# Kernel optimization log

Measured on AMD Instinct MI355X. Metric: run time of the kernel, lower is better.

The kernel has to match this reference:

```python
import jax, jax.numpy as jnp
import numpy as np

B, T, C, H = 2, 2048, 1024, 16
NS, NL, STEP = 3, 1, 8            # n_s_token, n_l_token, online_step
NPF = NS + NL                      # tokens per frame
CHUNK = STEP * NPF                 # online chunk size = 32
D = C // H


def _build_causal_mask():
    # Faithful port of the buffer construction in __init__ (host-side numpy).
    m = np.tril(np.ones((T, T), dtype=np.float32))
    step = np.zeros((T, T), dtype=np.float32)
    for i in range(0, T, CHUNK):
        step[i:i + CHUNK, i:i + CHUNK] = 1.0
        for j in range(i, i + CHUNK, NPF):
            m[j + NS:j + NPF, :] = 0.0
            m[:, j + NS:j + NPF] = 0.0
    return jnp.asarray(((m + step) == 0.0))[None, None]  # (1,1,T,T) bool


def setup_inputs() -> dict:
    key = jax.random.key(0)
    ks = jax.random.split(key, 10)
    sc = 0.02
    return {
        "x": jax.random.normal(ks[0], (B, T, C), dtype=jnp.float32),
        "dynamic_mask": jax.random.randint(ks[1], (B, 1, T, T), 0, 2).astype(bool),
        "causal_mask": _build_causal_mask(),
        "Wq": jax.random.normal(ks[2], (C, C), dtype=jnp.float32) * sc,
        "bq": jnp.zeros((C,), dtype=jnp.float32),
        "Wk": jax.random.normal(ks[3], (C, C), dtype=jnp.float32) * sc,
        "bk": jnp.zeros((C,), dtype=jnp.float32),
        "Wv": jax.random.normal(ks[4], (C, C), dtype=jnp.float32) * sc,
        "bv": jnp.zeros((C,), dtype=jnp.float32),
        "Wo": jax.random.normal(ks[5], (C, C), dtype=jnp.float32) * sc,
        "bo": jnp.zeros((C,), dtype=jnp.float32),
    }


def reference(x, dynamic_mask, causal_mask, Wq, bq, Wk, bk, Wv, bv, Wo, bo):
    Bb, Tt, Cc = x.shape
    scale = jnp.asarray(D, x.dtype) ** -0.5
    # nn.Linear: y = x @ W.T + b ; split heads -> (B,H,T,D)
    q = (x @ Wq.T + bq).reshape(Bb, Tt, H, D).transpose(0, 2, 1, 3)
    k = (x @ Wk.T + bk).reshape(Bb, Tt, H, D).transpose(0, 2, 1, 3)
    v = (x @ Wv.T + bv).reshape(Bb, Tt, H, D).transpose(0, 2, 1, 3)
    att = jnp.einsum('bhqd,bhkd->bhqk', q, k) * scale       # (B,H,T,T)
    neg_inf = jnp.asarray(-jnp.inf, att.dtype)
    att = jnp.where(causal_mask, neg_inf, att)
    att = jnp.where(dynamic_mask, neg_inf, att)
    att = jax.nn.softmax(att, axis=-1)                      # attn_drop is identity (eval)
    y = jnp.einsum('bhqk,bhkd->bhqd', att, v)
    y = y.transpose(0, 2, 1, 3).reshape(Bb, Tt, Cc)
    return y @ Wo.T + bo                                    # resid_drop is identity (eval)
```

## Files before the change

### kernel.cpp

```cpp
#include <hip/hip_runtime.h>

#define TSEQ 2048
#define NHEAD 16
#define DHEAD 64
#define CDIM 1024
#define BATCH 2

typedef __attribute__((ext_vector_type(8))) short bfx8;
typedef __attribute__((ext_vector_type(4))) short bfx4;
typedef __attribute__((ext_vector_type(4))) float f32x4;

__device__ __forceinline__ unsigned short f2bf(float f) {
  unsigned u = __builtin_bit_cast(unsigned, f);
  u += 0x7fffu + ((u >> 16) & 1u);
  return (unsigned short)(u >> 16);
}

__device__ __forceinline__ unsigned cvtpk(float lo, float hi) {
  unsigned r;
  asm("v_cvt_pk_bf16_f32 %0, %1, %2" : "=v"(r) : "v"(lo), "v"(hi));
  return r;
}

__device__ __forceinline__ float max3f(float a, float b, float c) {
  float d;
  asm("v_max3_f32 %0, %1, %2, %3" : "=v"(d) : "v"(a), "v"(b), "v"(c));
  return d;
}

__device__ __forceinline__ void gload16(const void* g, void* l) {
  __builtin_amdgcn_global_load_lds(
      (const __attribute__((address_space(1))) unsigned*)g,
      (__attribute__((address_space(3))) unsigned*)l, 16, 0, 0);
}

__global__ __launch_bounds__(256) void prep(
    const float* __restrict__ x,
    const float* __restrict__ wq, const float* __restrict__ wk,
    const float* __restrict__ wv, const float* __restrict__ wo,
    short* __restrict__ xb, short* __restrict__ wall,
    const unsigned char* __restrict__ dyn,
    const unsigned char* __restrict__ causal,
    unsigned long long* __restrict__ pm) {
  const int bid = blockIdx.x;
  if (bid < 20480) {
    const int y = bid >> 12;
    const float* src;
    short* dst;
    int n;
    if (y == 0) { src = x; dst = xb; n = (BATCH * TSEQ * CDIM) / 4; }
    else {
      src = (y == 1) ? wq : (y == 2) ? wk : (y == 3) ? wv : wo;
      dst = wall + (size_t)(y - 1) * CDIM * CDIM;
      n = (CDIM * CDIM) / 4;
    }
    const int i = (bid & 4095) * 256 + threadIdx.x;
    if (i < n) {
      const float4 v = ((const float4*)src)[i];
      bfx4 o;
      o[0] = (short)f2bf(v.x); o[1] = (short)f2bf(v.y);
      o[2] = (short)f2bf(v.z); o[3] = (short)f2bf(v.w);
      ((bfx4*)dst)[i] = o;
    }
  } else {
    const bool mbyte = (causal[32] != 0);
    const int wave = threadIdx.x >> 6, lane = threadIdx.x & 63;
    const int gid = (bid - 20480) * 4 + wave;
    const int tile = gid & 31;
    const int q = (gid >> 5) & (TSEQ - 1);
    const int b = gid >> 16;
    const int g = lane >> 4, blk = (lane >> 2) & 3, r = lane & 3;
    const int k = tile * 64 + blk * 16 + g * 4 + r;
    const size_t off = ((size_t)b * TSEQ + q) * TSEQ + k;
    const bool dm = mbyte ? (dyn[off] != 0) : (((const int*)dyn)[off] != 0);
    const bool qok = (q & 3) != 3;
    const bool al =
        (((k >> 5) == (q >> 5)) || ((k <= q) && qok && (r != 3))) && !dm;
    const unsigned long long bal = __ballot(!al);
    if (lane == 0) pm[gid] = bal;
  }
}

__global__ __launch_bounds__(256) void gemm_qkv(
    const short* __restrict__ A, const short* __restrict__ Ball,
    const float* __restrict__ bias0, const float* __restrict__ bias1,
    const float* __restrict__ bias2,
    short* __restrict__ Oq, short* __restrict__ Ok, short* __restrict__ VT) {
  __shared__ char arena[35072];
  const int bid = blockIdx.x;
  const int xcd = bid & 7, local = bid >> 3;
  const int m_idx = (xcd >> 1) * 8 + (local & 7);
  const int nz = (xcd & 1) * 12 + (local >> 3);
  const int which = nz >> 3, n_idx = nz & 7;
  const int tid = threadIdx.x;
  const int w = tid >> 6, lane = tid & 63;
  const int lq = lane & 15, g = lane >> 4;
  const int wr = w >> 1, wc = w & 1;
  const int m0 = m_idx * 128, n0 = n_idx * 128;
  const short* B = Ball + (size_t)which * CDIM * CDIM;
#define ASB(bi) ((short*)(arena + (bi) * 8192))
#define BSB(bi) ((short*)(arena + 16384 + (bi) * 8192))
#define GS(bi, kt)                                                             \
  {                                                                            \
    _Pragma("unroll") for (int ph = 0; ph < 2; ++ph) {                         \
      const int c = ph * 256 + tid;                                            \
      gload16(A + (size_t)(m0 + (c >> 2)) * CDIM + (kt) * 32 + (c & 3) * 8,    \
              ASB(bi) + (ph * 256 + w * 64) * 8);                              \
      gload16(B + (size_t)(n0 + (c >> 2)) * CDIM + (kt) * 32 + (c & 3) * 8,    \
              BSB(bi) + (ph * 256 + w * 64) * 8);                              \
    }                                                                          \
  }
  GS(0, 0);
  __syncthreads();
  f32x4 acc[4][4] = {};
#pragma unroll 2
  for (int kt = 0; kt < CDIM / 32; ++kt) {
    const int bi = kt & 1;
    if (kt + 1 < CDIM / 32) GS(bi ^ 1, kt + 1);
    bfx8 af[4], bfr[4];
#pragma unroll
    for (int i = 0; i < 4; ++i)
      af[i] = *(const bfx8*)&ASB(bi)[(wr * 64 + i * 16 + lq) * 32 + g * 8];
#pragma unroll
    for (int i = 0; i < 4; ++i)
      bfr[i] = *(const bfx8*)&BSB(bi)[(wc * 64 + i * 16 + lq) * 32 + g * 8];
#pragma unroll
    for (int i = 0; i < 4; ++i)
#pragma unroll
      for (int j = 0; j < 4; ++j)
        acc[i][j] = __builtin_amdgcn_mfma_f32_16x16x32_bf16(af[i], bfr[j],
                                                            acc[i][j], 0, 0, 0);
    __syncthreads();
  }
#undef GS
  const float* bias = (which == 0) ? bias0 : (which == 1) ? bias1 : bias2;
  const float scale = (which == 0) ? 0.18033688011112042f : 1.0f;
  short* tile = (short*)arena;
  const int rs = (which == 2) ? 137 : 136;
#pragma unroll
  for (int i = 0; i < 4; ++i)
#pragma unroll
    for (int j = 0; j < 4; ++j) {
      const int col = wc * 64 + j * 16 + lq;
      const float bb = bias[n0 + col];
#pragma unroll
      for (int r = 0; r < 4; ++r) {
        const int row = wr * 64 + i * 16 + g * 4 + r;
        tile[row * rs + col] = (short)f2bf((acc[i][j][r] + bb) * scale);
      }
    }
  __syncthreads();
  const int b_ = m0 >> 11, t0 = m0 & (TSEQ - 1);
  if (which == 2) {
#pragma unroll
    for (int it = 0; it < 8; ++it) {
      const int id = it * 256 + tid;
      const int tseg = id & 15, d128 = id >> 4;
      const int h = (n0 >> 6) + (d128 >> 6), d = d128 & 63;
      bfx8 o;
#pragma unroll
      for (int j = 0; j < 8; ++j) o[j] = tile[(tseg * 8 + j) * 137 + d128];
      *(bfx8*)&VT[(((size_t)b_ * NHEAD + h) * DHEAD + d) * TSEQ + t0 +
                  tseg * 8] = o;
    }
  } else {
    short* O = (which == 0) ? Oq : Ok;
#pragma unroll
    for (int it = 0; it < 8; ++it) {
      const int id = it * 256 + tid;
      const int m = id >> 4, c16 = id & 15;
      const int h = (n0 >> 6) + (c16 >> 3), d0 = (c16 & 7) * 8;
      *(bfx8*)&O[(((size_t)b_ * NHEAD + h) * TSEQ + t0 + m) * DHEAD + d0] =
          *(const bfx8*)&tile[m * 136 + c16 * 8];
    }
  }
}

__global__ __launch_bounds__(256) void gemm_out(
    const short* __restrict__ A, const short* __restrict__ B,
    const float* __restrict__ bias, float* __restrict__ Of) {
  __shared__ char arena[24576];
  const int bid = blockIdx.x;
  const int xcd = bid & 7, local = bid >> 3;
  const int m_idx = (xcd >> 1) * 16 + (local & 15);
  const int n_idx = (xcd & 1) * 4 + (local >> 4);
  const int tid = threadIdx.x;
  const int w = tid >> 6, lane = tid & 63;
  const int lq = lane & 15, g = lane >> 4;
  const int wr = w >> 1, wc = w & 1;
  const int m0 = m_idx * 64, n0 = n_idx * 128;
#define ASB(bi) ((short*)(arena + (bi) * 4096))
#define BSB(bi) ((short*)(arena + 8192 + (bi) * 8192))
#define GS(bi, kt)                                                             \
  {                                                                            \
    gload16(A + (size_t)(m0 + (tid >> 2)) * CDIM + (kt) * 32 + (tid & 3) * 8,  \
            ASB(bi) + (w * 64) * 8);                                           \
    _Pragma("unroll") for (int ph = 0; ph < 2; ++ph) {                         \
      const int c = ph * 256 + tid;                                            \
      gload16(B + (size_t)(n0 + (c >> 2)) * CDIM + (kt) * 32 + (c & 3) * 8,    \
              BSB(bi) + (ph * 256 + w * 64) * 8);                              \
    }                                                                          \
  }
  GS(0, 0);
  __syncthreads();
  f32x4 acc[2][4] = {};
#pragma unroll 2
  for (int kt = 0; kt < CDIM / 32; ++kt) {
    const int bi = kt & 1;
    if (kt + 1 < CDIM / 32) GS(bi ^ 1, kt + 1);
    bfx8 af[2], bfr[4];
#pragma unroll
    for (int i = 0; i < 2; ++i)
      af[i] = *(const bfx8*)&ASB(bi)[(wr * 32 + i * 16 + lq) * 32 + g * 8];
#pragma unroll
    for (int j = 0; j < 4; ++j)
      bfr[j] = *(const bfx8*)&BSB(bi)[(wc * 64 + j * 16 + lq) * 32 + g * 8];
#pragma unroll
    for (int i = 0; i < 2; ++i)
#pragma unroll
      for (int j = 0; j < 4; ++j)
        acc[i][j] = __builtin_amdgcn_mfma_f32_16x16x32_bf16(af[i], bfr[j],
                                                            acc[i][j], 0, 0, 0);
    __syncthreads();
  }
#undef GS
#undef ASB
#undef BSB
#pragma unroll
  for (int i = 0; i < 2; ++i)
#pragma unroll
    for (int j = 0; j < 4; ++j) {
      const int col = n0 + wc * 64 + j * 16 + lq;
      const float bb = bias[col];
#pragma unroll
      for (int r = 0; r < 4; ++r) {
        const int row = m0 + wr * 32 + i * 16 + g * 4 + r;
        Of[(size_t)row * CDIM + col] = acc[i][j][r] + bb;
      }
    }
}

struct QPhase {
  bfx8 qf0, qf1;
  f32x4 acc[4];
  float m, l;
  const unsigned short* pmr;
};

__device__ __forceinline__ void attn_half(QPhase& S, const char* kbuf,
                                          const char* vbuf, short* Pw,
                                          unsigned mb, int hf, int sw, int lq,
                                          int g) {
  f32x4 st[2] = {};
  __builtin_amdgcn_s_setprio(1);
#pragma unroll
  for (int b2 = 0; b2 < 2; ++b2) {
    const int rowb = ((hf * 2 + b2) * 16 + lq) * 128;
    const bfx8 kf0 = *(const bfx8*)&kbuf[rowb + ((g * 16) ^ sw)];
    const bfx8 kf1 = *(const bfx8*)&kbuf[rowb + ((64 + g * 16) ^ sw)];
    st[b2] =
        __builtin_amdgcn_mfma_f32_16x16x32_bf16(kf0, S.qf0, st[b2], 0, 0, 0);
    st[b2] =
        __builtin_amdgcn_mfma_f32_16x16x32_bf16(kf1, S.qf1, st[b2], 0, 0, 0);
  }
  __builtin_amdgcn_s_setprio(0);
  float s8[8];
#pragma unroll
  for (int idx = 0; idx < 8; ++idx)
    s8[idx] = ((mb >> idx) & 1u) ? -3.0e38f : st[idx >> 2][idx & 3];
  const float t0 = max3f(s8[0], s8[1], s8[2]);
  const float t1 = max3f(s8[3], s8[4], s8[5]);
  const float pmax = max3f(t0, t1, fmaxf(s8[6], s8[7]));
  if (!__all(pmax - S.m <= 8.f)) {
    float smax = fmaxf(pmax, __shfl_xor(pmax, 16));
    smax = fmaxf(smax, __shfl_xor(smax, 32));
    const float mnew = fmaxf(S.m, smax);
    const float fac = __builtin_amdgcn_exp2f(S.m - mnew);
    S.l *= fac;
    float fr[4];
#pragma unroll
    for (int r = 0; r < 4; ++r) fr[r] = __shfl(fac, g * 4 + r);
#pragma unroll
    for (int dc = 0; dc < 4; ++dc) {
      S.acc[dc][0] *= fr[0]; S.acc[dc][1] *= fr[1];
      S.acc[dc][2] *= fr[2]; S.acc[dc][3] *= fr[3];
    }
    S.m = mnew;
  }
  float psum = 0.f;
#pragma unroll
  for (int idx = 0; idx < 8; ++idx) {
    const float e = __builtin_amdgcn_exp2f(s8[idx] - S.m);
    s8[idx] = e;
    psum += e;
  }
  S.l += psum;
#pragma unroll
  for (int b2 = 0; b2 < 2; ++b2) {
    uint2 u;
    u.x = cvtpk(s8[b2 * 4 + 0], s8[b2 * 4 + 1]);
    u.y = cvtpk(s8[b2 * 4 + 2], s8[b2 * 4 + 3]);
    *(uint2*)&Pw[lq * 32 + b2 * 16 + g * 4] = u;
  }
  __builtin_amdgcn_wave_barrier();
  const bfx8 pa = *(const bfx8*)&Pw[lq * 32 + g * 8];
  __builtin_amdgcn_wave_barrier();
  __builtin_amdgcn_s_setprio(1);
#pragma unroll
  for (int dc = 0; dc < 4; ++dc) {
    const bfx8 vf = *(const bfx8*)&vbuf[(dc * 16 + lq) * 128 +
                                        ((hf * 64 + g * 16) ^ sw)];
    S.acc[dc] =
        __builtin_amdgcn_mfma_f32_16x16x32_bf16(pa, vf, S.acc[dc], 0, 0, 0);
  }
  __builtin_amdgcn_s_setprio(0);
}

__global__ __launch_bounds__(512, 8) void attn(
    const short* __restrict__ Q, const short* __restrict__ K,
    const short* __restrict__ VT, const unsigned short* __restrict__ pm,
    short* __restrict__ Y) {
  __shared__ char arena[40960];
  const int bid = blockIdx.x;
  const int x = bid & 255, y = bid >> 8;
  const int p = x >> 3;
  const int bh = (x & 7) * 4 + y;
  const int r5 = (p + 5) & 31;
  const int qb = (y == 0) ? p : (y == 1) ? (31 - p) : (y == 2) ? r5 : (31 - r5);
  const int tid = threadIdx.x;
  const int w = tid >> 6, lane = tid & 63;
  const int hf = w >> 2, ws = w & 3;
  const int lq = lane & 15, g = lane >> 4;
  const int b = bh >> 4, h = bh & 15;
  const short* Qb = Q + (size_t)bh * TSEQ * DHEAD;
  const short* Kb = K + (size_t)bh * TSEQ * DHEAD;
  const short* Vb = VT + (size_t)bh * DHEAD * TSEQ;

  QPhase S;
  {
    const int q = qb * 64 + ws * 16 + lq;
    S.qf0 = *(const bfx8*)(Qb + (size_t)q * DHEAD + g * 8);
    S.qf1 = *(const bfx8*)(Qb + (size_t)q * DHEAD + 32 + g * 8);
#pragma unroll
    for (int dc = 0; dc < 4; ++dc) S.acc[dc] = f32x4{};
    S.m = -1e30f;
    S.l = 0.f;
    S.pmr = pm + ((size_t)(b * TSEQ + q) << 7) + g;
  }

  const int sl = lane >> 3, sc = lane & 7;
  const int ssw = (sc ^ sl) * 8;
  const int sw = (lq & 7) << 4;
  short* Pw = (short*)(arena + 32768 + w * 1024);

#define STAGE(bufn, k0s)                                                      \
  {                                                                           \
    gload16(Kb + (size_t)((k0s) + w * 8 + sl) * DHEAD + ssw,                  \
            arena + (bufn) * 16384 + w * 1024);                               \
    gload16(Vb + (size_t)(w * 8 + sl) * TSEQ + (k0s) + ssw,                   \
            arena + (bufn) * 16384 + 8192 + w * 1024);                        \
  }

#define PHASE(t, BUF)                                                         \
  {                                                                           \
    const unsigned pmw = S.pmr[(t) << 2];                                     \
    __builtin_amdgcn_sched_barrier(0);                                        \
    if ((t) < qb) STAGE((BUF) ^ 1, ((t) + 1) * 64);                           \
    const char* kbuf_ = arena + (BUF) * 16384;                                \
    const char* vbuf_ = kbuf_ + 8192;                                         \
    attn_half(S, kbuf_, vbuf_, Pw, (pmw >> (hf * 8)) & 0xffu, hf, sw, lq, g); \
    __syncthreads();                                                          \
  }

  STAGE(0, 0);
  __syncthreads();

  int t = 0;
  for (; t + 1 <= qb; t += 2) {
    PHASE(t, 0);
    PHASE(t + 1, 1);
  }
  if (t <= qb) PHASE(t, 0);
#undef PHASE
#undef STAGE

  float* exA = (float*)arena;
  float2* exM = (float2*)(arena + 16384);
  if (hf == 1) {
    float* a = exA + ws * 1024;
#pragma unroll
    for (int dc = 0; dc < 4; ++dc) *(f32x4*)&a[lane * 16 + dc * 4] = S.acc[dc];
    exM[ws * 64 + lane] = float2{S.m, S.l};
  }
  __syncthreads();
  if (hf == 0) {
    const float* a = exA + ws * 1024;
    const float2 mlB = exM[ws * 64 + lane];
    const float ms = fmaxf(S.m, mlB.x);
    const float fA = __builtin_amdgcn_exp2f(S.m - ms);
    const float fB = __builtin_amdgcn_exp2f(mlB.x - ms);
    float lr = S.l * fA + mlB.y * fB;
    lr += __shfl_xor(lr, 16);
    lr += __shfl_xor(lr, 32);
    float frA[4], frB[4], li[4];
#pragma unroll
    for (int r = 0; r < 4; ++r) {
      frA[r] = __shfl(fA, g * 4 + r);
      frB[r] = __shfl(fB, g * 4 + r);
      const float lv = __shfl(lr, g * 4 + r);
      li[r] = lv > 0.f ? 1.f / lv : 0.f;
    }
    const int q0 = qb * 64 + ws * 16;
#pragma unroll
    for (int dc = 0; dc < 4; ++dc) {
      const f32x4 ab = *(const f32x4*)&a[lane * 16 + dc * 4];
#pragma unroll
      for (int r = 0; r < 4; ++r) {
        const int t2 = q0 + g * 4 + r;
        Y[((size_t)b * TSEQ + t2) * CDIM + h * DHEAD + dc * 16 + lq] =
            (short)f2bf((S.acc[dc][r] * frA[r] + ab[r] * frB[r]) * li[r]);
      }
    }
  }
}

extern "C" void kernel_launch(void* const* d_in, const int* in_sizes, int n_in,
                              void* d_out, int out_size, void* d_ws,
                              size_t ws_size, hipStream_t stream) {
  const float* x = (const float*)d_in[0];
  const unsigned char* dyn = (const unsigned char*)d_in[1];
  const unsigned char* causal = (const unsigned char*)d_in[2];
  const float* Wq = (const float*)d_in[3];
  const float* bq = (const float*)d_in[4];
  const float* Wk = (const float*)d_in[5];
  const float* bk = (const float*)d_in[6];
  const float* Wv = (const float*)d_in[7];
  const float* bv = (const float*)d_in[8];
  const float* Wo = (const float*)d_in[9];
  const float* bo = (const float*)d_in[10];

  char* ws = (char*)d_ws;
  const size_t MB8 = 8ull * 1024 * 1024;
  short* xb = (short*)(ws + 0 * MB8);
  short* wall = (short*)(ws + 1 * MB8);
  short* Qb = (short*)(ws + 2 * MB8);
  short* Kb = (short*)(ws + 3 * MB8);
  short* VTb = (short*)(ws + 5 * MB8);
  short* Yb = (short*)(ws + 6 * MB8);
  unsigned long long* pmask = (unsigned long long*)(ws + 7 * MB8);

  prep<<<dim3(53248), 256, 0, stream>>>(x, Wq, Wk, Wv, Wo, xb, wall, dyn,
                                        causal, pmask);
  gemm_qkv<<<dim3(768), 256, 0, stream>>>(xb, wall, bq, bk, bv, Qb, Kb, VTb);
  attn<<<dim3(1024), 512, 0, stream>>>(Qb, Kb, VTb,
                                       (const unsigned short*)pmask, Yb);
  gemm_out<<<dim3(512), 256, 0, stream>>>(Yb, wall + 3 * CDIM * CDIM, bo,
                                          (float*)d_out);
}
```

Before: 143.6 us.

## Trim prep grid, pad P scratch rows, retune attn occupancy and block mapping

The prep kernel stops launching idle blocks for the weight conversion: the earlier grid reserved 4096 blocks per weight matrix but only needed 1024. Each mask-packing wave now handles four rows instead of one, which shrinks the grid. In attention, the per-wave P scratch row stride is padded from 32 to 40 shorts to reduce LDS bank conflicts, and LDS grows to match. The launch-bounds occupancy hint drops from 8 to 4, and the block-to-(head, q-block) mapping is simplified to alternate forward and reversed q order to balance causal work per XCD.

```diff
diff --git a/kernel.cpp b/kernel.cpp
--- a/kernel.cpp
+++ b/kernel.cpp
@@ -43,41 +43,46 @@
     const unsigned char* __restrict__ causal,
     unsigned long long* __restrict__ pm) {
   const int bid = blockIdx.x;
-  if (bid < 20480) {
-    const int y = bid >> 12;
+  if (bid < 8192) {
     const float* src;
     short* dst;
-    int n;
-    if (y == 0) { src = x; dst = xb; n = (BATCH * TSEQ * CDIM) / 4; }
-    else {
-      src = (y == 1) ? wq : (y == 2) ? wk : (y == 3) ? wv : wo;
-      dst = wall + (size_t)(y - 1) * CDIM * CDIM;
-      n = (CDIM * CDIM) / 4;
-    }
-    const int i = (bid & 4095) * 256 + threadIdx.x;
-    if (i < n) {
-      const float4 v = ((const float4*)src)[i];
-      bfx4 o;
-      o[0] = (short)f2bf(v.x); o[1] = (short)f2bf(v.y);
-      o[2] = (short)f2bf(v.z); o[3] = (short)f2bf(v.w);
-      ((bfx4*)dst)[i] = o;
-    }
+    int i;
+    if (bid < 4096) {
+      src = x;
+      dst = xb;
+      i = bid * 256 + threadIdx.x;
+    } else {
+      const int wsel = (bid - 4096) >> 10;
+      src = (wsel == 0) ? wq : (wsel == 1) ? wk : (wsel == 2) ? wv : wo;
+      dst = wall + (size_t)wsel * CDIM * CDIM;
+      i = ((bid - 4096) & 1023) * 256 + threadIdx.x;
+    }
+    const float4 v = ((const float4*)src)[i];
+    bfx4 o;
+    o[0] = (short)f2bf(v.x); o[1] = (short)f2bf(v.y);
+    o[2] = (short)f2bf(v.z); o[3] = (short)f2bf(v.w);
+    ((bfx4*)dst)[i] = o;
   } else {
     const bool mbyte = (causal[32] != 0);
     const int wave = threadIdx.x >> 6, lane = threadIdx.x & 63;
-    const int gid = (bid - 20480) * 4 + wave;
-    const int tile = gid & 31;
-    const int q = (gid >> 5) & (TSEQ - 1);
-    const int b = gid >> 16;
     const int g = lane >> 4, blk = (lane >> 2) & 3, r = lane & 3;
-    const int k = tile * 64 + blk * 16 + g * 4 + r;
-    const size_t off = ((size_t)b * TSEQ + q) * TSEQ + k;
-    const bool dm = mbyte ? (dyn[off] != 0) : (((const int*)dyn)[off] != 0);
-    const bool qok = (q & 3) != 3;
-    const bool al =
-        (((k >> 5) == (q >> 5)) || ((k <= q) && qok && (r != 3))) && !dm;
-    const unsigned long long bal = __ballot(!al);
-    if (lane == 0) pm[gid] = bal;
+    const int kl = blk * 16 + g * 4 + r;
+    const bool rok = (r != 3);
+#pragma unroll
+    for (int j = 0; j < 4; ++j) {
+      const int gid = (bid - 8192) * 16 + wave * 4 + j;
+      const int tile = gid & 31;
+      const int q = (gid >> 5) & (TSEQ - 1);
+      const int b = gid >> 16;
+      const int k = tile * 64 + kl;
+      const size_t off = ((size_t)b * TSEQ + q) * TSEQ + k;
+      const bool dm = mbyte ? (dyn[off] != 0) : (((const int*)dyn)[off] != 0);
+      const bool qok = (q & 3) != 3;
+      const bool al =
+          (((k >> 5) == (q >> 5)) || ((k <= q) && qok && rok)) && !dm;
+      const unsigned long long bal = __ballot(!al);
+      if (lane == 0) pm[gid] = bal;
+    }
   }
 }
 
@@ -300,10 +305,10 @@
     uint2 u;
     u.x = cvtpk(s8[b2 * 4 + 0], s8[b2 * 4 + 1]);
     u.y = cvtpk(s8[b2 * 4 + 2], s8[b2 * 4 + 3]);
-    *(uint2*)&Pw[lq * 32 + b2 * 16 + g * 4] = u;
+    *(uint2*)&Pw[lq * 40 + b2 * 16 + g * 4] = u;
   }
   __builtin_amdgcn_wave_barrier();
-  const bfx8 pa = *(const bfx8*)&Pw[lq * 32 + g * 8];
+  const bfx8 pa = *(const bfx8*)&Pw[lq * 40 + g * 8];
   __builtin_amdgcn_wave_barrier();
   __builtin_amdgcn_s_setprio(1);
 #pragma unroll
@@ -316,17 +321,16 @@
   __builtin_amdgcn_s_setprio(0);
 }
 
-__global__ __launch_bounds__(512, 8) void attn(
+__global__ __launch_bounds__(512, 4) void attn(
     const short* __restrict__ Q, const short* __restrict__ K,
     const short* __restrict__ VT, const unsigned short* __restrict__ pm,
     short* __restrict__ Y) {
-  __shared__ char arena[40960];
+  __shared__ char arena[43008];
   const int bid = blockIdx.x;
-  const int x = bid & 255, y = bid >> 8;
-  const int p = x >> 3;
-  const int bh = (x & 7) * 4 + y;
-  const int r5 = (p + 5) & 31;
-  const int qb = (y == 0) ? p : (y == 1) ? (31 - p) : (y == 2) ? r5 : (31 - r5);
+  const int local = bid >> 3;
+  const int u = local & 31, v = local >> 5;
+  const int bh = (bid & 7) * 4 + v;
+  const int qb = (v & 1) ? (31 - u) : u;
   const int tid = threadIdx.x;
   const int w = tid >> 6, lane = tid & 63;
   const int hf = w >> 2, ws = w & 3;
@@ -351,7 +355,7 @@
   const int sl = lane >> 3, sc = lane & 7;
   const int ssw = (sc ^ sl) * 8;
   const int sw = (lq & 7) << 4;
-  short* Pw = (short*)(arena + 32768 + w * 1024);
+  short* Pw = (short*)(arena + 32768 + w * 1280);
 
 #define STAGE(bufn, k0s)                                                      \
   {                                                                           \
@@ -449,7 +453,7 @@
   short* Yb = (short*)(ws + 6 * MB8);
   unsigned long long* pmask = (unsigned long long*)(ws + 7 * MB8);
 
-  prep<<<dim3(53248), 256, 0, stream>>>(x, Wq, Wk, Wv, Wo, xb, wall, dyn,
+  prep<<<dim3(16384), 256, 0, stream>>>(x, Wq, Wk, Wv, Wo, xb, wall, dyn,
                                         causal, pmask);
   gemm_qkv<<<dim3(768), 256, 0, stream>>>(xb, wall, bq, bk, bv, Qb, Kb, VTb);
   attn<<<dim3(1024), 512, 0, stream>>>(Qb, Kb, VTb,
```

Result: faster. 125.2 us (-12.8%).
